# Performance work log

Hardware: AMD Instinct MI355X
Metric: run time of the kernel (lower is better)

Reference implementation:

```python
import jax, jax.numpy as jnp
import numpy as np

H = 128  # hidden_dim


def setup_inputs() -> dict:
    key = jax.random.key(0)
    k1, k2, k3 = jax.random.split(key, 3)
    N = 1024
    return {
        "node_emb": jax.random.normal(k1, (N, H), dtype=jnp.float32),
        "W1": jax.random.normal(k2, (2 * H, H), dtype=jnp.float32) * 0.05,
        "b1": jnp.zeros((H,), dtype=jnp.float32),
        "W2": jax.random.normal(k3, (H, 1), dtype=jnp.float32) * 0.05,
        "b2": jnp.zeros((1,), dtype=jnp.float32),
    }


def reference(node_emb, W1, b1, W2, b2):
    # L2 normalize rows (torch F.normalize: x / max(||x||, eps))
    norm = jnp.sqrt(jnp.sum(node_emb * node_emb, axis=-1, keepdims=True))
    e = node_emb / jnp.maximum(norm, 1e-12)  # (N, H)
    # adj[i, j] = mlp(cat(e_i, e_j)); split W1 so we never materialize (N,N,2H)
    left = e @ W1[:H]    # (N, H) contribution of e_i
    right = e @ W1[H:]   # (N, H) contribution of e_j
    h = jax.nn.relu(left[:, None, :] + right[None, :, :] + b1)  # (N, N, H)
    logits = jnp.einsum("ijh,h->ij", h, W2[:, 0]) + b2[0]       # (N, N)
    return jax.nn.softmax(logits, axis=-1)
```

## Files before the change

### kernel.cpp

```cpp
#include <hip/hip_runtime.h>

#define H 128
#define N 1024
#define SLOTS 144

__global__ __launch_bounds__(512) void prep_kernel(
    const float* __restrict__ x, const float* __restrict__ W1,
    const float* __restrict__ b1, const float* __restrict__ W2,
    float* __restrict__ LpS, float* __restrict__ Rt,
    float* __restrict__ c, int* __restrict__ meta)
{
    constexpr int PF = 16;
    __shared__ float e_s[4][H];
    __shared__ float cred[4][2];
    __shared__ int   slot_s[H];
    __shared__ int   cnt_s[2];
    __shared__ int   meta_s[3];
    __shared__ float4 stageL[SLOTS];
    __shared__ float4 stageR[SLOTS];
    const int t = threadIdx.x;
    const int i0 = blockIdx.x * 4;

    bool pos = false; int rank = 0;
    if (t < H) {
        const int lane = t & 63;
        pos = (W2[t] >= 0.f);
        const unsigned long long bal = __ballot(pos);
        rank = __popcll(bal & ((1ull << lane) - 1ull));
        if (lane == 0) cnt_s[t >> 6] = __popcll(bal);
    }
    if (t < 256) {
        const int row = t >> 6, lane = t & 63;
        const float2 v = *reinterpret_cast<const float2*>(&x[(i0 + row) * H + 2 * lane]);
        float s = v.x * v.x + v.y * v.y;
#pragma unroll
        for (int off = 32; off; off >>= 1) s += __shfl_xor(s, off);
        const float rn = 1.0f / fmaxf(sqrtf(s), 1e-12f);
        e_s[row][2 * lane]     = v.x * rn;
        e_s[row][2 * lane + 1] = v.y * rn;
    }
    __syncthreads();

    if (t < H) {
        const int c0 = cnt_s[0];
        const int P  = c0 + cnt_s[1];
        const int P8 = (P + 7) & ~7;
        const int lane = t & 63;
        int slot;
        if (pos) slot = (t < 64 ? 0 : c0) + rank;
        else     slot = P8 + (t < 64 ? 0 : 64 - c0) + (lane - rank);
        slot_s[t] = slot;
        if (t == 0) {
            meta_s[0] = P8;
            meta_s[1] = P8 + ((H - P + 7) & ~7);
            meta_s[2] = P;
        }
    }
    __syncthreads();

    const int h = t & (H - 1);
    const int q = t >> 7;
    const int r0 = (q & 1) * 2;
    const float* Wb = W1 + (q >= 2 ? H * H : 0) + h;

    float acc0 = 0.f, acc1 = 0.f;
    float wbuf[PF];
#pragma unroll
    for (int p = 0; p < PF; ++p) wbuf[p] = Wb[p * H];

    for (int kb = 0; kb < H - PF; kb += PF) {
#pragma unroll
        for (int p = 0; p < PF; ++p) {
            const float w = wbuf[p];
            wbuf[p] = Wb[(kb + p + PF) * H];
            acc0 = fmaf(e_s[r0][kb + p],     w, acc0);
            acc1 = fmaf(e_s[r0 + 1][kb + p], w, acc1);
        }
    }
#pragma unroll
    for (int p = 0; p < PF; ++p) {
        const int k = H - PF + p;
        acc0 = fmaf(e_s[r0][k],     wbuf[p], acc0);
        acc1 = fmaf(e_s[r0 + 1][k], wbuf[p], acc1);
    }

    const float w2h = W2[h];
    const int slot = slot_s[h];
    float* stg = q < 2 ? (float*)&stageL[slot] : (float*)&stageR[slot];
    if (q < 2) {
        const float bb = b1[h];
        stg[r0]     = w2h * (acc0 + bb);
        stg[r0 + 1] = w2h * (acc1 + bb);
    } else {
        const float v0 = w2h * acc0, v1 = w2h * acc1;
        stg[r0]     = v0;
        stg[r0 + 1] = v1;
        float s0 = v0, s1 = v1;
#pragma unroll
        for (int off = 32; off; off >>= 1) {
            s0 += __shfl_xor(s0, off);
            s1 += __shfl_xor(s1, off);
        }
        const int wv = t >> 6;
        if ((t & 63) == 0) { cred[wv - 4][0] = s0; cred[wv - 4][1] = s1; }
    }
    {
        const int P8m = meta_s[0], T8m = meta_s[1], Pm = meta_s[2];
        const float4 z = {0.f, 0.f, 0.f, 0.f};
        if (t >= 64 && t < 72) {
            const int k = t - 64;
            if (k < P8m - Pm) { stageL[Pm + k] = z; stageR[Pm + k] = z; }
        } else if (t >= 72 && t < 80) {
            const int k = t - 72;
            const int base2 = P8m + (H - Pm);
            if (k < T8m - base2) { stageL[base2 + k] = z; stageR[base2 + k] = z; }
        }
    }
    __syncthreads();

    const int T8 = meta_s[1];
    if (t < 4)
        c[i0 + t] = cred[(t >> 1) * 2][t & 1] + cred[(t >> 1) * 2 + 1][t & 1];
    if (t < T8)
        *reinterpret_cast<float4*>(&LpS[t * N + i0]) = stageL[t];
    else if (t >= 256 && t < 256 + T8)
        *reinterpret_cast<float4*>(&Rt[(t - 256) * N + i0]) = stageR[t - 256];
    if (blockIdx.x == 0 && t == 0) { meta[0] = meta_s[0]; meta[1] = meta_s[1]; }
}

__global__ __launch_bounds__(1024) void adj_kernel(
    const float* __restrict__ LpS, const float* __restrict__ Rt,
    const float* __restrict__ c, const int* __restrict__ meta,
    float* __restrict__ out)
{
    constexpr int II = 4;
    __shared__ float4 LsT[SLOTS];
    __shared__ float red_m[II][16];
    __shared__ float red_s[II][16];

    const int t = threadIdx.x;
    const int lane = t & 63, wave = t >> 6;
    const int i0 = blockIdx.x * II;

    const int P8 = meta[0], T8 = meta[1];

    if (t < T8)
        LsT[t] = *reinterpret_cast<const float4*>(&LpS[t * N + i0]);
    const float cj = c[t];
    __syncthreads();

    float acc[II];
#pragma unroll
    for (int ii = 0; ii < II; ++ii) acc[ii] = cj;

    const float* Rp = Rt + t;
    float rbuf[8];
#pragma unroll
    for (int p = 0; p < 8; ++p) rbuf[p] = Rp[p * N];

    int hb = 0;
    for (; hb < P8; hb += 8) {
#pragma unroll
        for (int p = 0; p < 8; ++p) {
            const int s = hb + p;
            const float r = rbuf[p];
            rbuf[p] = Rp[(s + 8) * N];
            const float4 lv = LsT[s];
            const float* lp = &lv.x;
#pragma unroll
            for (int ii = 0; ii < II; ++ii) acc[ii] += fabsf(lp[ii] + r);
        }
    }
    for (; hb < T8; hb += 8) {
#pragma unroll
        for (int p = 0; p < 8; ++p) {
            const int s = hb + p;
            const float r = rbuf[p];
            rbuf[p] = Rp[(s + 8) * N];
            const float4 lv = LsT[s];
            const float* lp = &lv.x;
#pragma unroll
            for (int ii = 0; ii < II; ++ii) acc[ii] -= fabsf(lp[ii] + r);
        }
    }

#pragma unroll
    for (int ii = 0; ii < II; ++ii) acc[ii] *= 0.5f;

#pragma unroll
    for (int ii = 0; ii < II; ++ii) {
        float m = acc[ii];
#pragma unroll
        for (int off = 32; off; off >>= 1) m = fmaxf(m, __shfl_xor(m, off));
        if (lane == 0) red_m[ii][wave] = m;
    }
    __syncthreads();

    float mm[II];
#pragma unroll
    for (int ii = 0; ii < II; ++ii) {
        float m = red_m[ii][0];
#pragma unroll
        for (int w = 1; w < 16; ++w) m = fmaxf(m, red_m[ii][w]);
        mm[ii] = m;
    }

#pragma unroll
    for (int ii = 0; ii < II; ++ii) {
        acc[ii] = expf(acc[ii] - mm[ii]);
        float s = acc[ii];
#pragma unroll
        for (int off = 32; off; off >>= 1) s += __shfl_xor(s, off);
        if (lane == 0) red_s[ii][wave] = s;
    }
    __syncthreads();

#pragma unroll
    for (int ii = 0; ii < II; ++ii) {
        float s = red_s[ii][0];
#pragma unroll
        for (int w = 1; w < 16; ++w) s += red_s[ii][w];
        out[(i0 + ii) * N + t] = acc[ii] * (1.0f / s);
    }
}

extern "C" void kernel_launch(void* const* d_in, const int* in_sizes, int n_in,
                              void* d_out, int out_size, void* d_ws, size_t ws_size,
                              hipStream_t stream) {
    const float* x  = (const float*)d_in[0];
    const float* W1 = (const float*)d_in[1];
    const float* b1 = (const float*)d_in[2];
    const float* W2 = (const float*)d_in[3];
    float* out = (float*)d_out;

    float* wsf = (float*)d_ws;
    float* LpS = wsf;
    float* Rt  = LpS + SLOTS * N;
    float* cc  = Rt + SLOTS * N;
    int*   meta = (int*)(cc + N);

    prep_kernel<<<N / 4, 512, 0, stream>>>(x, W1, b1, W2, LpS, Rt, cc, meta);
    adj_kernel<<<N / 4, 1024, 0, stream>>>(LpS, Rt, cc, meta, out);
}
```

Measured before the change: 30.22 us.

## Register-tile adjacency kernel over 4 columns per thread with fixed slot loop

The adjacency kernel now runs 256 threads per block, and each thread computes a 4x4 tile of rows and columns. It loads R values as float4 and reuses each shared L vector across four columns, which cuts shared-memory reads per output. The two sign-dependent loops are merged into one fixed-count loop (136 slots) that multiplies by a per-group sign, and the zero padding now always extends to 136 slots. The cost is fewer waves per CU, so there is less latency hiding for the strided global loads of R.

```diff
diff --git a/kernel.cpp b/kernel.cpp
--- a/kernel.cpp
+++ b/kernel.cpp
@@ -2,7 +2,8 @@
 
 #define H 128
 #define N 1024
-#define SLOTS 144
+#define SLOTS 136
+#define SLOTS_A 144
 
 __global__ __launch_bounds__(512) void prep_kernel(
     const float* __restrict__ x, const float* __restrict__ W1,
@@ -15,7 +16,7 @@
     __shared__ float cred[4][2];
     __shared__ int   slot_s[H];
     __shared__ int   cnt_s[2];
-    __shared__ int   meta_s[3];
+    __shared__ int   meta_s[2];
     __shared__ float4 stageL[SLOTS];
     __shared__ float4 stageR[SLOTS];
     const int t = threadIdx.x;
@@ -50,11 +51,7 @@
         if (pos) slot = (t < 64 ? 0 : c0) + rank;
         else     slot = P8 + (t < 64 ? 0 : 64 - c0) + (lane - rank);
         slot_s[t] = slot;
-        if (t == 0) {
-            meta_s[0] = P8;
-            meta_s[1] = P8 + ((H - P + 7) & ~7);
-            meta_s[2] = P;
-        }
+        if (t == 0) { meta_s[0] = P8; meta_s[1] = P; }
     }
     __syncthreads();
 
@@ -105,7 +102,7 @@
         if ((t & 63) == 0) { cred[wv - 4][0] = s0; cred[wv - 4][1] = s1; }
     }
     {
-        const int P8m = meta_s[0], T8m = meta_s[1], Pm = meta_s[2];
+        const int P8m = meta_s[0], Pm = meta_s[1];
         const float4 z = {0.f, 0.f, 0.f, 0.f};
         if (t >= 64 && t < 72) {
             const int k = t - 64;
@@ -113,83 +110,78 @@
         } else if (t >= 72 && t < 80) {
             const int k = t - 72;
             const int base2 = P8m + (H - Pm);
-            if (k < T8m - base2) { stageL[base2 + k] = z; stageR[base2 + k] = z; }
-        }
-    }
-    __syncthreads();
-
-    const int T8 = meta_s[1];
+            if (k < SLOTS - base2) { stageL[base2 + k] = z; stageR[base2 + k] = z; }
+        }
+    }
+    __syncthreads();
+
     if (t < 4)
         c[i0 + t] = cred[(t >> 1) * 2][t & 1] + cred[(t >> 1) * 2 + 1][t & 1];
-    if (t < T8)
+    if (t < SLOTS)
         *reinterpret_cast<float4*>(&LpS[t * N + i0]) = stageL[t];
-    else if (t >= 256 && t < 256 + T8)
+    else if (t >= 256 && t < 256 + SLOTS)
         *reinterpret_cast<float4*>(&Rt[(t - 256) * N + i0]) = stageR[t - 256];
-    if (blockIdx.x == 0 && t == 0) { meta[0] = meta_s[0]; meta[1] = meta_s[1]; }
+    if (blockIdx.x == 0 && t == 0) meta[0] = meta_s[0];
 }
 
-__global__ __launch_bounds__(1024) void adj_kernel(
+__global__ __launch_bounds__(256) void adj_kernel(
     const float* __restrict__ LpS, const float* __restrict__ Rt,
     const float* __restrict__ c, const int* __restrict__ meta,
     float* __restrict__ out)
 {
-    constexpr int II = 4;
+    constexpr int II = 4, JJ = 4;
     __shared__ float4 LsT[SLOTS];
-    __shared__ float red_m[II][16];
-    __shared__ float red_s[II][16];
+    __shared__ float red_m[II][4];
+    __shared__ float red_s[II][4];
 
     const int t = threadIdx.x;
     const int lane = t & 63, wave = t >> 6;
     const int i0 = blockIdx.x * II;
-
-    const int P8 = meta[0], T8 = meta[1];
-
-    if (t < T8)
+    const int j0 = t * JJ;
+
+    const int P8 = meta[0];
+
+    if (t < SLOTS)
         LsT[t] = *reinterpret_cast<const float4*>(&LpS[t * N + i0]);
-    const float cj = c[t];
-    __syncthreads();
-
-    float acc[II];
-#pragma unroll
-    for (int ii = 0; ii < II; ++ii) acc[ii] = cj;
-
-    const float* Rp = Rt + t;
-    float rbuf[8];
-#pragma unroll
-    for (int p = 0; p < 8; ++p) rbuf[p] = Rp[p * N];
-
-    int hb = 0;
-    for (; hb < P8; hb += 8) {
+    const float4 cj = *reinterpret_cast<const float4*>(&c[j0]);
+    __syncthreads();
+
+    float acc[II][JJ];
+    const float* cjp = &cj.x;
+#pragma unroll
+    for (int ii = 0; ii < II; ++ii)
+#pragma unroll
+        for (int jj = 0; jj < JJ; ++jj) acc[ii][jj] = 0.5f * cjp[jj];
+
+    const float* Rp = Rt + j0;
+    float4 rbuf[8];
+#pragma unroll
+    for (int p = 0; p < 8; ++p)
+        rbuf[p] = *reinterpret_cast<const float4*>(&Rp[p * N]);
+
+#pragma unroll 1
+    for (int g = 0; g < SLOTS / 8; ++g) {
+        const float sg = (8 * g < P8) ? 0.5f : -0.5f;
 #pragma unroll
         for (int p = 0; p < 8; ++p) {
-            const int s = hb + p;
-            const float r = rbuf[p];
-            rbuf[p] = Rp[(s + 8) * N];
+            const int s = 8 * g + p;
+            const float4 r = rbuf[p];
+            rbuf[p] = *reinterpret_cast<const float4*>(&Rp[(s + 8) * N]);
             const float4 lv = LsT[s];
             const float* lp = &lv.x;
-#pragma unroll
-            for (int ii = 0; ii < II; ++ii) acc[ii] += fabsf(lp[ii] + r);
-        }
-    }
-    for (; hb < T8; hb += 8) {
-#pragma unroll
-        for (int p = 0; p < 8; ++p) {
-            const int s = hb + p;
-            const float r = rbuf[p];
-            rbuf[p] = Rp[(s + 8) * N];
-            const float4 lv = LsT[s];
-            const float* lp = &lv.x;
-#pragma unroll
-            for (int ii = 0; ii < II; ++ii) acc[ii] -= fabsf(lp[ii] + r);
-        }
-    }
-
-#pragma unroll
-    for (int ii = 0; ii < II; ++ii) acc[ii] *= 0.5f;
+            const float* rp = &r.x;
+#pragma unroll
+            for (int ii = 0; ii < II; ++ii)
+#pragma unroll
+                for (int jj = 0; jj < JJ; ++jj)
+                    acc[ii][jj] = fmaf(sg, fabsf(lp[ii] + rp[jj]), acc[ii][jj]);
+        }
+    }
 
 #pragma unroll
     for (int ii = 0; ii < II; ++ii) {
-        float m = acc[ii];
+        float m = fmaxf(fmaxf(acc[ii][0], acc[ii][1]),
+                        fmaxf(acc[ii][2], acc[ii][3]));
 #pragma unroll
         for (int off = 32; off; off >>= 1) m = fmaxf(m, __shfl_xor(m, off));
         if (lane == 0) red_m[ii][wave] = m;
@@ -198,17 +190,18 @@
 
     float mm[II];
 #pragma unroll
+    for (int ii = 0; ii < II; ++ii)
+        mm[ii] = fmaxf(fmaxf(red_m[ii][0], red_m[ii][1]),
+                       fmaxf(red_m[ii][2], red_m[ii][3]));
+
+#pragma unroll
     for (int ii = 0; ii < II; ++ii) {
-        float m = red_m[ii][0];
-#pragma unroll
-        for (int w = 1; w < 16; ++w) m = fmaxf(m, red_m[ii][w]);
-        mm[ii] = m;
-    }
-
-#pragma unroll
-    for (int ii = 0; ii < II; ++ii) {
-        acc[ii] = expf(acc[ii] - mm[ii]);
-        float s = acc[ii];
+        float s = 0.f;
+#pragma unroll
+        for (int jj = 0; jj < JJ; ++jj) {
+            acc[ii][jj] = expf(acc[ii][jj] - mm[ii]);
+            s += acc[ii][jj];
+        }
 #pragma unroll
         for (int off = 32; off; off >>= 1) s += __shfl_xor(s, off);
         if (lane == 0) red_s[ii][wave] = s;
@@ -217,10 +210,12 @@
 
 #pragma unroll
     for (int ii = 0; ii < II; ++ii) {
-        float s = red_s[ii][0];
-#pragma unroll
-        for (int w = 1; w < 16; ++w) s += red_s[ii][w];
-        out[(i0 + ii) * N + t] = acc[ii] * (1.0f / s);
+        const float s = red_s[ii][0] + red_s[ii][1] + red_s[ii][2] + red_s[ii][3];
+        const float rcp = 1.0f / s;
+        float4 o;
+        o.x = acc[ii][0] * rcp; o.y = acc[ii][1] * rcp;
+        o.z = acc[ii][2] * rcp; o.w = acc[ii][3] * rcp;
+        *reinterpret_cast<float4*>(&out[(i0 + ii) * N + j0]) = o;
     }
 }
 
@@ -235,10 +230,10 @@
 
     float* wsf = (float*)d_ws;
     float* LpS = wsf;
-    float* Rt  = LpS + SLOTS * N;
-    float* cc  = Rt + SLOTS * N;
+    float* Rt  = LpS + SLOTS_A * N;
+    float* cc  = Rt + SLOTS_A * N;
     int*   meta = (int*)(cc + N);
 
     prep_kernel<<<N / 4, 512, 0, stream>>>(x, W1, b1, W2, LpS, Rt, cc, meta);
-    adj_kernel<<<N / 4, 1024, 0, stream>>>(LpS, Rt, cc, meta, out);
+    adj_kernel<<<N / 4, 256, 0, stream>>>(LpS, Rt, cc, meta, out);
 }
```

Measured after the change: 33.16 us. +9.7%, slower.
